# Optimization experiments

Measured on AMD Instinct MI355X. Metric: run time of the kernel, lower is better.

Reference implementation:

```python
import jax, jax.numpy as jnp
import numpy as np

B, N, E = 32, 128, 16384
D, H, O, A = 72, 72, 72, 4   # n_input, n_hidden, n_output, n_node_attr
C_WEIGHT = 1.0
EPS = 1e-5  # BatchNorm1d default eps


def setup_inputs() -> dict:
    key = jax.random.key(0)
    ks = jax.random.split(key, 16)
    rn = lambda k, shp, s=0.05: jax.random.normal(k, shp, jnp.float32) * s
    return {
        "h": jax.random.normal(ks[0], (B, N, D), jnp.float32),
        "x": jax.random.normal(ks[1], (B, N, 4), jnp.float32),
        "edgei": jax.random.randint(ks[2], (B, E), 0, N),
        "edgej": jax.random.randint(ks[3], (B, E), 0, N),
        "node_attr": jax.random.normal(ks[4], (B, N, A), jnp.float32),
        # phi_e: Linear(2D+2 -> H, no bias), BN, ReLU, Linear(H->H), ReLU
        "We1": rn(ks[5], (2 * D + 2, H)),
        "g1": jnp.ones((H,), jnp.float32), "b1": jnp.zeros((H,), jnp.float32),
        "We2": rn(ks[6], (H, H)), "be2": jnp.zeros((H,), jnp.float32),
        # phi_m: Linear(H->1), Sigmoid
        "Wm": rn(ks[7], (H, 1)), "bm": jnp.zeros((1,), jnp.float32),
        # phi_x: Linear(H->H), ReLU, Linear(H->1, no bias, tiny init)
        "Wx1": rn(ks[8], (H, H)), "bx1": jnp.zeros((H,), jnp.float32),
        "Wx2": rn(ks[9], (H, 1), 0.001),
        # phi_h: Linear(H+D+A -> H), BN, ReLU, Linear(H->O)
        "Wh1": rn(ks[10], (H + D + A, H)), "bh1": jnp.zeros((H,), jnp.float32),
        "gh": jnp.ones((H,), jnp.float32), "bh": jnp.zeros((H,), jnp.float32),
        "Wh2": rn(ks[11], (H, O)), "bh2": jnp.zeros((O,), jnp.float32),
    }


def _psi(p):
    return jnp.sign(p) * jnp.log1p(jnp.abs(p))


def _normsq4(p):  # Minkowski norm: p0^2 - p1^2 - p2^2 - p3^2
    psq = p * p
    return 2.0 * psq[..., 0] - psq.sum(axis=-1)


def _dotsq4(p, q):  # Minkowski inner product
    pq = p * q
    return 2.0 * pq[..., 0] - pq.sum(axis=-1)


def _batchnorm(z, g, b):  # training-mode BatchNorm1d over flattened batch dim
    mu = z.mean(axis=0)
    var = z.var(axis=0)
    return (z - mu) * jax.lax.rsqrt(var + EPS) * g + b


_seg_sum = jax.vmap(lambda d, s: jax.ops.segment_sum(d, s, num_segments=N))


def reference(h, x, edgei, edgej, node_attr,
              We1, g1, b1, We2, be2, Wm, bm,
              Wx1, bx1, Wx2, Wh1, bh1, gh, bh, Wh2, bh2):
    # gather edge endpoint features (equiv. to torch.gather along dim 1)
    xi = jnp.take_along_axis(x, edgei[:, :, None], axis=1)    # [B,E,4]
    xj = jnp.take_along_axis(x, edgej[:, :, None], axis=1)
    hi = jnp.take_along_axis(h, edgei[:, :, None], axis=1)    # [B,E,D]
    hj = jnp.take_along_axis(h, edgej[:, :, None], axis=1)
    x_diff = xi - xj
    norms = _psi(_normsq4(x_diff))[..., None]                 # [B,E,1]
    dots = _psi(_dotsq4(xi, xj))[..., None]                   # [B,E,1]

    # m_model: phi_e then sigmoid gate phi_m
    feat = jnp.concatenate([hi, hj, norms, dots], axis=-1)    # [B,E,2D+2]
    z = feat.reshape(-1, 2 * D + 2) @ We1
    z = jax.nn.relu(_batchnorm(z, g1, b1))
    z = jax.nn.relu(z @ We2 + be2)
    m = z.reshape(B, E, H)
    m = m * jax.nn.sigmoid(m @ Wm + bm)                       # gated messages

    # x_model: equivariant coordinate update (segment mean over edges)
    gate = jax.nn.relu(m @ Wx1 + bx1) @ Wx2                   # [B,E,1]
    trans = jnp.clip(x_diff * gate, -100.0, 100.0)
    agg = _seg_sum(trans, edgei)                              # [B,N,4]
    cnt = _seg_sum(jnp.ones_like(trans), edgei)
    x_out = x + (agg / jnp.maximum(cnt, 1.0)) * C_WEIGHT

    # h_model: segment sum of messages, node MLP, residual
    magg = _seg_sum(m, edgei)                                 # [B,N,H]
    hin = jnp.concatenate([h, magg, node_attr], axis=-1).reshape(-1, H + D + A)
    z2 = hin @ Wh1 + bh1
    z2 = jax.nn.relu(_batchnorm(z2, gh, bh))
    z2 = z2 @ Wh2 + bh2
    h_out = h + z2.reshape(B, N, O)

    return (h_out, x_out, m)
```

## Files before the change

kernel.cpp:

```cpp
#include <hip/hip_runtime.h>

#define BB 32
#define NN 128
#define EE 16384
#define ROWS_E (BB*EE)
#define ROWS_N (BB*NN)
#define EPS_BN 1e-5f

#define XOUT_OFF (ROWS_N*72)
#define M_OFF    (XOUT_OFF + ROWS_N*4)

#define ST1_OFF 0
#define ST2_OFF 512
#define AGG_OFF 1024
#define CNT_OFF (AGG_OFF + ROWS_N*4)
#define MAGG_OFF (CNT_OFF + ROWS_N)
#define Z2_OFF (MAGG_OFF + ROWS_N*72)
#define WB_OFF (Z2_OFF + ROWS_N*72)

#define WE1T_OFF 0
#define WE2T_OFF 13440
#define WX1T_OFF 21760
#define WH1T_OFF 30080
#define WH2T_OFF 43520
#define WB_TOTAL 51840
#define WAB_TOTAL 13824
#define PREP_TOTAL (WB_TOTAL + WAB_TOTAL)

typedef __attribute__((ext_vector_type(8))) short short8;
typedef __attribute__((ext_vector_type(4))) float f32x4;

__device__ __forceinline__ float psi_f(float p) {
    return copysignf(log1pf(fabsf(p)), p);
}
__device__ __forceinline__ unsigned pk(float a, float b) {
    unsigned r;
    asm("v_cvt_pk_bf16_f32 %0, %1, %2" : "=v"(r) : "v"(a), "v"(b));
    return r;
}
__device__ __forceinline__ unsigned short f2bf(float f) {
    unsigned r;
    asm("v_cvt_pk_bf16_f32 %0, %1, %1" : "=v"(r) : "v"(f));
    return (unsigned short)r;
}

__global__ void k_prep(const float* __restrict__ We1, const float* __restrict__ We2,
                       const float* __restrict__ Wx1, const float* __restrict__ Wh1,
                       const float* __restrict__ Wh2, unsigned short* __restrict__ wb,
                       unsigned short* __restrict__ wab)
{
    int idx = blockIdx.x * 256 + threadIdx.x;
    if (idx >= PREP_TOTAL) return;
    if (idx >= WB_TOTAL) {
        int off = idx - WB_TOTAL, n = off / 96, k = off % 96;
        float v = 0.f;
        if (k < 72) v = (n < 72) ? We1[k * 72 + n] : We1[(72 + k) * 72 + (n - 72)];
        wab[off] = f2bf(v);
        return;
    }
    const float* src; int off, n, k, K;
    if (idx < WE2T_OFF)      { off = idx;            n = off/168; k = off%168; src = We1; K = 146; }
    else if (idx < WH1T_OFF && idx >= WX1T_OFF) { off = idx - WX1T_OFF; n = off/104; k = off%104; src = Wx1; K = 72; }
    else if (idx < WX1T_OFF) { off = idx - WE2T_OFF; n = off/104; k = off%104; src = We2; K = 72; }
    else if (idx < WH2T_OFF) { off = idx - WH1T_OFF; n = off/168; k = off%168; src = Wh1; K = 148; }
    else                     { off = idx - WH2T_OFF; n = off/104; k = off%104; src = Wh2; K = 72; }
    float v = (n < 72 && k < K) ? src[k * 72 + n] : 0.f;
    wb[idx] = f2bf(v);
}

__global__ __launch_bounds__(256, 2) void k_ab(
    const float* __restrict__ h, const unsigned short* __restrict__ Wabt,
    float* __restrict__ ab)
{
    __shared__ unsigned short Hs[128 * 104];
    int tid = threadIdx.x;
    int rl = tid >> 1, half = tid & 1;
    size_t row = (size_t)blockIdx.x * 128 + rl;
    const float4* hp = (const float4*)(h + row * 72) + half * 9;
    uint2* hr = (uint2*)(&Hs[rl * 104 + half * 36]);
    #pragma unroll
    for (int q = 0; q < 9; q++) {
        float4 v = hp[q];
        hr[q] = make_uint2(pk(v.x, v.y), pk(v.z, v.w));
    }
    {
        uint2* zp = (uint2*)(&Hs[rl * 104 + 72 + half * 12]);
        zp[0] = make_uint2(0u, 0u); zp[1] = make_uint2(0u, 0u); zp[2] = make_uint2(0u, 0u);
    }
    int wv = tid >> 6, lane = tid & 63, c = lane & 15, quad = lane >> 4;
    f32x4 acc[2][9] = {};
    #pragma unroll
    for (int kc = 0; kc < 3; kc++) {
        int k0 = kc * 32 + quad * 8;
        short8 a0 = *(const short8*)(&Hs[(wv * 32 + c) * 104 + k0]);
        short8 a1 = *(const short8*)(&Hs[(wv * 32 + 16 + c) * 104 + k0]);
        #pragma unroll
        for (int ct = 0; ct < 9; ct++) {
            short8 bf = *(const short8*)(&Wabt[(ct * 16 + c) * 96 + k0]);
            acc[0][ct] = __builtin_amdgcn_mfma_f32_16x16x32_bf16(a0, bf, acc[0][ct], 0, 0, 0);
            acc[1][ct] = __builtin_amdgcn_mfma_f32_16x16x32_bf16(a1, bf, acc[1][ct], 0, 0, 0);
        }
    }
    size_t rbase = (size_t)blockIdx.x * 128 + wv * 32 + quad * 4;
    #pragma unroll
    for (int rt = 0; rt < 2; rt++)
        #pragma unroll
        for (int ct = 0; ct < 9; ct++) {
            int col = ct * 16 + c;
            #pragma unroll
            for (int r = 0; r < 4; r++)
                ab[(rbase + rt * 16 + r) * 144 + col] = acc[rt][ct][r];
        }
}

__global__ __launch_bounds__(288) void k_stats_lite(
    const float* __restrict__ ab, const float* __restrict__ x,
    const int* __restrict__ ei, const int* __restrict__ ej,
    const float* __restrict__ We1, float* __restrict__ st)
{
    __shared__ float uu[256], tt[256];
    __shared__ int iofs[256], jofs[256];
    __shared__ float ssum[4][72];
    __shared__ float ssq[4][72];
    int c = threadIdx.x, ty = threadIdx.y;
    int tf = ty * 72 + c;
    float al = We1[144 * 72 + c], be = We1[145 * 72 + c];
    float s = 0.f, q = 0.f;
    int ebase = blockIdx.x * 512;
    #pragma unroll
    for (int tile = 0; tile < 2; tile++) {
        if (tf < 256) {
            int e = ebase + tile * 256 + tf;
            int b = e >> 14;
            int i = ei[e], j = ej[e];
            float4 xi = *(const float4*)(x + (size_t)(b * 128 + i) * 4);
            float4 xj = *(const float4*)(x + (size_t)(b * 128 + j) * 4);
            float d0 = xi.x - xj.x, d1 = xi.y - xj.y, d2 = xi.z - xj.z, d3 = xi.w - xj.w;
            uu[tf] = psi_f(d0*d0 - d1*d1 - d2*d2 - d3*d3);
            tt[tf] = psi_f(xi.x*xj.x - xi.y*xj.y - xi.z*xj.z - xi.w*xj.w);
            iofs[tf] = (b * 128 + i) * 144;
            jofs[tf] = (b * 128 + j) * 144 + 72;
        }
        __syncthreads();
        #pragma unroll 4
        for (int k = 0; k < 64; k++) {
            int idx = ty * 64 + k;
            float av = ab[iofs[idx] + c];
            float bv = ab[jofs[idx] + c];
            float z = (av + bv) + (uu[idx] * al + tt[idx] * be);
            s += z; q += z * z;
        }
        __syncthreads();
    }
    ssum[ty][c] = s; ssq[ty][c] = q;
    __syncthreads();
    if (ty == 0) {
        s = ssum[0][c] + ssum[1][c] + ssum[2][c] + ssum[3][c];
        q = ssq[0][c] + ssq[1][c] + ssq[2][c] + ssq[3][c];
        atomicAdd(&st[c], s);
        atomicAdd(&st[72 + c], q);
    }
}

__global__ void k_finalize1(float* __restrict__ st, const float* __restrict__ g1,
                            const float* __restrict__ b1, float inv_rows)
{
    int c = threadIdx.x;
    if (c < 72) {
        float mean = st[c] * inv_rows;
        float var  = st[72 + c] * inv_rows - mean * mean;
        float sc = rsqrtf(var + EPS_BN) * g1[c];
        st[144 + c] = sc;
        st[216 + c] = b1[c] - mean * sc;
    }
}

__global__ void k_finalize(float* __restrict__ st, float inv_rows)
{
    int c = threadIdx.x;
    if (c < 72) {
        float mean = st[c] * inv_rows;
        float var  = st[72 + c] * inv_rows - mean * mean;
        st[144 + c] = mean;
        st[216 + c] = rsqrtf(var + EPS_BN);
    }
}

__global__ __launch_bounds__(256, 4) void k_edge_fused(
    const float* __restrict__ ab, const float* __restrict__ x,
    const int* __restrict__ ei, const int* __restrict__ ej,
    const float* __restrict__ We1, const float* __restrict__ st1,
    const float* __restrict__ be2, const float* __restrict__ Wm, const float* __restrict__ bm,
    const float* __restrict__ bx1, const float* __restrict__ Wx2,
    const unsigned short* __restrict__ We2t, const unsigned short* __restrict__ Wx1t,
    float* __restrict__ m, float* __restrict__ agg, float* __restrict__ cnt)
{
    __shared__ unsigned short Zt[128 * 104];
    __shared__ float g2buf[128];
    int tid = threadIdx.x;
    int rl = tid >> 1, half = tid & 1;
    size_t row = (size_t)blockIdx.x * 128 + rl;
    int b = (int)(row >> 14);
    int i = ei[row], j = ej[row];
    float4 xi = *(const float4*)(x + (size_t)(b * 128 + i) * 4);
    float4 xj = *(const float4*)(x + (size_t)(b * 128 + j) * 4);
    float d0 = xi.x - xj.x, d1 = xi.y - xj.y, d2 = xi.z - xj.z, d3 = xi.w - xj.w;
    float u = psi_f(d0*d0 - d1*d1 - d2*d2 - d3*d3);
    float t = psi_f(xi.x*xj.x - xi.y*xj.y - xi.z*xj.z - xi.w*xj.w);
    const float4* ar  = (const float4*)(ab + (size_t)(b * 128 + i) * 144 + half * 36);
    const float4* br  = (const float4*)(ab + (size_t)(b * 128 + j) * 144 + 72 + half * 36);
    const float4* alp = (const float4*)(We1 + 144 * 72 + half * 36);
    const float4* bep = (const float4*)(We1 + 145 * 72 + half * 36);
    const float4* scp = (const float4*)(st1 + 144 + half * 36);
    const float4* shp = (const float4*)(st1 + 216 + half * 36);
    uint2* zrow = (uint2*)(&Zt[rl * 104 + half * 36]);
    #pragma unroll
    for (int q = 0; q < 9; q++) {
        float4 av = ar[q], bv = br[q], al = alp[q], be = bep[q], sc = scp[q], sh = shp[q];
        float z0 = fmaxf((av.x + bv.x + u * al.x + t * be.x) * sc.x + sh.x, 0.f);
        float z1 = fmaxf((av.y + bv.y + u * al.y + t * be.y) * sc.y + sh.y, 0.f);
        float z2 = fmaxf((av.z + bv.z + u * al.z + t * be.z) * sc.z + sh.z, 0.f);
        float z3 = fmaxf((av.w + bv.w + u * al.w + t * be.w) * sc.w + sh.w, 0.f);
        zrow[q] = make_uint2(pk(z0, z1), pk(z2, z3));
    }
    {
        uint2* zp = (uint2*)(&Zt[rl * 104 + 72 + half * 12]);
        zp[0] = make_uint2(0u, 0u); zp[1] = make_uint2(0u, 0u); zp[2] = make_uint2(0u, 0u);
    }

    int wv = tid >> 6, lane = tid & 63, c = lane & 15, quad = lane >> 4;
    f32x4 acc2[2][5] = {};
    #pragma unroll
    for (int kc = 0; kc < 3; kc++) {
        int k0 = kc * 32 + quad * 8;
        short8 a0 = *(const short8*)(&Zt[(wv * 32 + c) * 104 + k0]);
        short8 a1 = *(const short8*)(&Zt[(wv * 32 + 16 + c) * 104 + k0]);
        #pragma unroll
        for (int ct = 0; ct < 5; ct++) {
            short8 bf = *(const short8*)(&We2t[(ct * 16 + c) * 104 + k0]);
            acc2[0][ct] = __builtin_amdgcn_mfma_f32_16x16x32_bf16(a0, bf, acc2[0][ct], 0, 0, 0);
            acc2[1][ct] = __builtin_amdgcn_mfma_f32_16x16x32_bf16(a1, bf, acc2[1][ct], 0, 0, 0);
        }
    }
    float part[2][4] = {};
    float bm0 = bm[0];
    #pragma unroll
    for (int ct = 0; ct < 5; ct++) {
        int col = ct * 16 + c;
        float bias = (col < 72) ? be2[col] : 0.f;
        float wm   = (col < 72) ? Wm[col]  : 0.f;
        #pragma unroll
        for (int rt = 0; rt < 2; rt++)
            #pragma unroll
            for (int r = 0; r < 4; r++) {
                float tv = fmaxf(acc2[rt][ct][r] + bias, 0.f);
                acc2[rt][ct][r] = tv;
                part[rt][r] += tv * wm;
            }
    }
    float sg[2][4];
    #pragma unroll
    for (int rt = 0; rt < 2; rt++)
        #pragma unroll
        for (int r = 0; r < 4; r++) {
            float s = part[rt][r];
            s += __shfl_xor(s, 1); s += __shfl_xor(s, 2);
            s += __shfl_xor(s, 4); s += __shfl_xor(s, 8);
            sg[rt][r] = 1.f / (1.f + expf(-(s + bm0)));
        }
    size_t rbase = (size_t)blockIdx.x * 128 + wv * 32 + quad * 4;
    #pragma unroll
    for (int rt = 0; rt < 2; rt++)
        #pragma unroll
        for (int ct = 0; ct < 5; ct++) {
            int col = ct * 16 + c;
            #pragma unroll
            for (int r = 0; r < 4; r++) {
                float mv = acc2[rt][ct][r] * sg[rt][r];
                int lrow = wv * 32 + rt * 16 + quad * 4 + r;
                Zt[lrow * 104 + col] = f2bf(mv);
                if (col < 72) m[(rbase + rt * 16 + r) * 72 + col] = mv;
            }
        }
    f32x4 acc3[2][5] = {};
    #pragma unroll
    for (int kc = 0; kc < 3; kc++) {
        int k0 = kc * 32 + quad * 8;
        short8 a0 = *(const short8*)(&Zt[(wv * 32 + c) * 104 + k0]);
        short8 a1 = *(const short8*)(&Zt[(wv * 32 + 16 + c) * 104 + k0]);
        #pragma unroll
        for (int ct = 0; ct < 5; ct++) {
            short8 bf = *(const short8*)(&Wx1t[(ct * 16 + c) * 104 + k0]);
            acc3[0][ct] = __builtin_amdgcn_mfma_f32_16x16x32_bf16(a0, bf, acc3[0][ct], 0, 0, 0);
            acc3[1][ct] = __builtin_amdgcn_mfma_f32_16x16x32_bf16(a1, bf, acc3[1][ct], 0, 0, 0);
        }
    }
    float part3[2][4] = {};
    #pragma unroll
    for (int ct = 0; ct < 5; ct++) {
        int col = ct * 16 + c;
        float bias = (col < 72) ? bx1[col] : 0.f;
        float wx   = (col < 72) ? Wx2[col] : 0.f;
        #pragma unroll
        for (int rt = 0; rt < 2; rt++)
            #pragma unroll
            for (int r = 0; r < 4; r++)
                part3[rt][r] += fmaxf(acc3[rt][ct][r] + bias, 0.f) * wx;
    }
    #pragma unroll
    for (int rt = 0; rt < 2; rt++)
        #pragma unroll
        for (int r = 0; r < 4; r++) {
            float s = part3[rt][r];
            s += __shfl_xor(s, 1); s += __shfl_xor(s, 2);
            s += __shfl_xor(s, 4); s += __shfl_xor(s, 8);
            if (c == 0) g2buf[wv * 32 + rt * 16 + quad * 4 + r] = s;
        }
    __syncthreads();
    if (tid < 128) {
        size_t erow = (size_t)blockIdx.x * 128 + tid;
        int b2 = (int)(erow >> 14);
        int i2 = ei[erow], j2 = ej[erow];
        float g2 = g2buf[tid];
        float4 xi2 = *(const float4*)(x + (size_t)(b2 * 128 + i2) * 4);
        float4 xj2 = *(const float4*)(x + (size_t)(b2 * 128 + j2) * 4);
        float t0 = fminf(fmaxf((xi2.x - xj2.x) * g2, -100.f), 100.f);
        float t1 = fminf(fmaxf((xi2.y - xj2.y) * g2, -100.f), 100.f);
        float t2 = fminf(fmaxf((xi2.z - xj2.z) * g2, -100.f), 100.f);
        float t3 = fminf(fmaxf((xi2.w - xj2.w) * g2, -100.f), 100.f);
        float* ap = agg + (size_t)(b2 * 128 + i2) * 4;
        atomicAdd(ap + 0, t0); atomicAdd(ap + 1, t1);
        atomicAdd(ap + 2, t2); atomicAdd(ap + 3, t3);
        atomicAdd(cnt + (size_t)(b2 * 128 + i2), 1.f);
    }
}

__global__ __launch_bounds__(256, 4) void k_magg(
    const float* __restrict__ m, const int* __restrict__ ei, float* __restrict__ magg)
{
    __shared__ float accum[128 * 72];
    int tid = threadIdx.x;
    for (int q = tid; q < 9216; q += 256) accum[q] = 0.f;
    __syncthreads();
    int b = blockIdx.x >> 5, chunk = blockIdx.x & 31;
    int wv = tid >> 6, lane = tid & 63;
    int ebase = b * 16384 + chunk * 512;
    for (int e = wv; e < 512; e += 8) {
        int e0 = ebase + e, e1 = ebase + e + 4;
        int n0 = ei[e0], n1 = ei[e1];
        const float* r0 = m + (size_t)e0 * 72;
        const float* r1 = m + (size_t)e1 * 72;
        float v0 = r0[lane];
        float v1 = r1[lane];
        float t0 = (lane < 8) ? r0[64 + lane] : 0.f;
        float t1 = (lane < 8) ? r1[64 + lane] : 0.f;
        atomicAdd(&accum[n0 * 72 + lane], v0);
        if (lane < 8) atomicAdd(&accum[n0 * 72 + 64 + lane], t0);
        atomicAdd(&accum[n1 * 72 + lane], v1);
        if (lane < 8) atomicAdd(&accum[n1 * 72 + 64 + lane], t1);
    }
    __syncthreads();
    float* mg = magg + (size_t)b * 9216;
    for (int q = tid; q < 9216; q += 256) atomicAdd(&mg[q], accum[q]);
}

__global__ __launch_bounds__(256) void k_node_gemm1(
    const float* __restrict__ h, const float* __restrict__ node_attr,
    const float* __restrict__ magg, const unsigned short* __restrict__ Wh1t,
    const float* __restrict__ bh1, float* __restrict__ z2, float* __restrict__ st)
{
    __shared__ unsigned short At[128 * 168];
    __shared__ unsigned short Wt[80 * 168];
    __shared__ float sred[4][144];
    int tid = threadIdx.x;
    {
        const uint4* s = (const uint4*)Wh1t; uint4* d = (uint4*)Wt;
        for (int q = tid; q < 1680; q += 256) d[q] = s[q];
    }
    int rl = tid >> 1, half = tid & 1;
    size_t row = (size_t)blockIdx.x * 128 + rl;
    const float4* sp = (const float4*)((half ? magg : h) + row * 72);
    uint2* arow = (uint2*)(&At[rl * 168 + half * 72]);
    #pragma unroll
    for (int q = 0; q < 18; q++) {
        float4 v = sp[q];
        arow[q] = make_uint2(pk(v.x, v.y), pk(v.z, v.w));
    }
    if (half) {
        float4 na = *(const float4*)(node_attr + row * 4);
        *(unsigned*)(&At[rl * 168 + 144]) = pk(na.x, na.y);
        *(unsigned*)(&At[rl * 168 + 146]) = pk(na.z, na.w);
        unsigned* tailp = (unsigned*)(&At[rl * 168 + 148]);
        #pragma unroll
        for (int q = 0; q < 10; q++) tailp[q] = 0u;
    }
    __syncthreads();

    int wv = tid >> 6, lane = tid & 63, c = lane & 15, quad = lane >> 4;
    f32x4 acc[2][5] = {};
    #pragma unroll
    for (int kc = 0; kc < 5; kc++) {
        int k0 = kc * 32 + quad * 8;
        short8 a0 = *(const short8*)(&At[(wv * 32 + c) * 168 + k0]);
        short8 a1 = *(const short8*)(&At[(wv * 32 + 16 + c) * 168 + k0]);
        #pragma unroll
        for (int ct = 0; ct < 5; ct++) {
            short8 bf = *(const short8*)(&Wt[(ct * 16 + c) * 168 + k0]);
            acc[0][ct] = __builtin_amdgcn_mfma_f32_16x16x32_bf16(a0, bf, acc[0][ct], 0, 0, 0);
            acc[1][ct] = __builtin_amdgcn_mfma_f32_16x16x32_bf16(a1, bf, acc[1][ct], 0, 0, 0);
        }
    }
    size_t rbase = (size_t)blockIdx.x * 128 + wv * 32 + quad * 4;
    #pragma unroll
    for (int ct = 0; ct < 5; ct++) {
        int col = ct * 16 + c;
        float bias = (col < 72) ? bh1[col] : 0.f;
        float s = 0.f, q = 0.f;
        #pragma unroll
        for (int rt = 0; rt < 2; rt++) {
            float* op = z2 + (rbase + rt * 16) * 72 + col;
            #pragma unroll
            for (int r = 0; r < 4; r++) {
                float v = acc[rt][ct][r] + bias;
                if (col < 72) op[(size_t)r * 72] = v;
                s += v; q += v * v;
            }
        }
        s += __shfl_xor(s, 16); s += __shfl_xor(s, 32);
        q += __shfl_xor(q, 16); q += __shfl_xor(q, 32);
        if (lane < 16 && col < 72) { sred[wv][col] = s; sred[wv][72 + col] = q; }
    }
    __syncthreads();
    if (tid < 144)
        atomicAdd(&st[tid], sred[0][tid] + sred[1][tid] + sred[2][tid] + sred[3][tid]);
}

__global__ __launch_bounds__(256) void k_node_final(
    const float* __restrict__ h, const float* __restrict__ x,
    const float* __restrict__ z2, const float* __restrict__ st2,
    const float* __restrict__ gh, const float* __restrict__ bh,
    const unsigned short* __restrict__ Wh2t, const float* __restrict__ bh2,
    const float* __restrict__ agg, const float* __restrict__ cnt,
    float* __restrict__ hout, float* __restrict__ xout)
{
    __shared__ unsigned short Zt[128 * 104];
    __shared__ unsigned short Wt[80 * 104];
    int tid = threadIdx.x;
    {
        const uint4* s = (const uint4*)Wh2t; uint4* d = (uint4*)Wt;
        for (int q = tid; q < 1040; q += 256) d[q] = s[q];
    }
    int rl = tid >> 1, half = tid & 1;
    size_t row = (size_t)blockIdx.x * 128 + rl;
    const float* mean = st2 + 144;
    const float* inv  = st2 + 216;
    const float4* zp = (const float4*)(z2 + row * 72) + half * 9;
    uint2* arow = (uint2*)(&Zt[rl * 104 + half * 36]);
    #pragma unroll
    for (int q = 0; q < 9; q++) {
        int k = half * 36 + q * 4;
        float4 v = zp[q];
        float a0 = fmaxf((v.x - mean[k  ]) * inv[k  ] * gh[k  ] + bh[k  ], 0.f);
        float a1 = fmaxf((v.y - mean[k+1]) * inv[k+1] * gh[k+1] + bh[k+1], 0.f);
        float a2 = fmaxf((v.z - mean[k+2]) * inv[k+2] * gh[k+2] + bh[k+2], 0.f);
        float a3 = fmaxf((v.w - mean[k+3]) * inv[k+3] * gh[k+3] + bh[k+3], 0.f);
        arow[q] = make_uint2(pk(a0, a1), pk(a2, a3));
    }
    uint2* prow = (uint2*)(&Zt[rl * 104]);
    #pragma unroll
    for (int q = 0; q < 4; q++) prow[18 + half * 4 + q] = make_uint2(0u, 0u);
    __syncthreads();

    int wv = tid >> 6, lane = tid & 63, c = lane & 15, quad = lane >> 4;
    f32x4 acc[2][5] = {};
    #pragma unroll
    for (int kc = 0; kc < 3; kc++) {
        int k0 = kc * 32 + quad * 8;
        short8 a0 = *(const short8*)(&Zt[(wv * 32 + c) * 104 + k0]);
        short8 a1 = *(const short8*)(&Zt[(wv * 32 + 16 + c) * 104 + k0]);
        #pragma unroll
        for (int ct = 0; ct < 5; ct++) {
            short8 bf = *(const short8*)(&Wt[(ct * 16 + c) * 104 + k0]);
            acc[0][ct] = __builtin_amdgcn_mfma_f32_16x16x32_bf16(a0, bf, acc[0][ct], 0, 0, 0);
            acc[1][ct] = __builtin_amdgcn_mfma_f32_16x16x32_bf16(a1, bf, acc[1][ct], 0, 0, 0);
        }
    }
    size_t rbase = (size_t)blockIdx.x * 128 + wv * 32 + quad * 4;
    #pragma unroll
    for (int rt = 0; rt < 2; rt++)
        #pragma unroll
        for (int ct = 0; ct < 5; ct++) {
            int col = ct * 16 + c;
            if (col < 72) {
                float bias = bh2[col];
                #pragma unroll
                for (int r = 0; r < 4; r++) {
                    size_t gr = (rbase + rt * 16 + r);
                    hout[gr * 72 + col] = h[gr * 72 + col] + acc[rt][ct][r] + bias;
                }
            }
        }
    if (tid < 128) {
        size_t nrow = (size_t)blockIdx.x * 128 + tid;
        float cn = fmaxf(cnt[nrow], 1.f);
        float4 ag = *(const float4*)(agg + nrow * 4);
        float4 xv = *(const float4*)(x + nrow * 4);
        ((float4*)xout)[nrow] = make_float4(xv.x + ag.x / cn, xv.y + ag.y / cn,
                                            xv.z + ag.z / cn, xv.w + ag.w / cn);
    }
}

extern "C" void kernel_launch(void* const* d_in, const int* in_sizes, int n_in,
                              void* d_out, int out_size, void* d_ws, size_t ws_size,
                              hipStream_t stream)
{
    const float* h   = (const float*)d_in[0];
    const float* x   = (const float*)d_in[1];
    const int*   ei  = (const int*)d_in[2];
    const int*   ej  = (const int*)d_in[3];
    const float* na  = (const float*)d_in[4];
    const float* We1 = (const float*)d_in[5];
    const float* g1  = (const float*)d_in[6];
    const float* b1  = (const float*)d_in[7];
    const float* We2 = (const float*)d_in[8];
    const float* be2 = (const float*)d_in[9];
    const float* Wm  = (const float*)d_in[10];
    const float* bm  = (const float*)d_in[11];
    const float* Wx1 = (const float*)d_in[12];
    const float* bx1 = (const float*)d_in[13];
    const float* Wx2 = (const float*)d_in[14];
    const float* Wh1 = (const float*)d_in[15];
    const float* bh1 = (const float*)d_in[16];
    const float* gh  = (const float*)d_in[17];
    const float* bhp = (const float*)d_in[18];
    const float* Wh2 = (const float*)d_in[19];
    const float* bh2 = (const float*)d_in[20];

    float* out  = (float*)d_out;
    float* hout = out;
    float* xout = out + XOUT_OFF;
    float* m    = out + M_OFF;
    float* ws   = (float*)d_ws;
    float* st1  = ws + ST1_OFF;
    float* st2  = ws + ST2_OFF;
    float* agg  = ws + AGG_OFF;
    float* cnt  = ws + CNT_OFF;
    float* magg = ws + MAGG_OFF;
    float* z2   = ws + Z2_OFF;
    unsigned short* wb = (unsigned short*)(ws + WB_OFF);
    float* ab = ws + MAGG_OFF;
    unsigned short* wab = (unsigned short*)xout;

    hipMemsetAsync(d_ws, 0, (size_t)MAGG_OFF * sizeof(float), stream);
    k_prep<<<(PREP_TOTAL + 255) / 256, 256, 0, stream>>>(We1, We2, Wx1, Wh1, Wh2, wb, wab);
    k_ab<<<ROWS_N / 128, 256, 0, stream>>>(h, wab, ab);
    k_stats_lite<<<1024, dim3(72, 4), 0, stream>>>(ab, x, ei, ej, We1, st1);
    k_finalize1<<<1, 128, 0, stream>>>(st1, g1, b1, 1.0f / (float)ROWS_E);
    k_edge_fused<<<ROWS_E / 128, 256, 0, stream>>>(ab, x, ei, ej, We1, st1, be2, Wm, bm,
                                                   bx1, Wx2, wb + WE2T_OFF, wb + WX1T_OFF,
                                                   m, agg, cnt);
    hipMemsetAsync(magg, 0, (size_t)(ROWS_N * 72) * sizeof(float), stream);
    k_magg<<<1024, 256, 0, stream>>>(m, ei, magg);
    k_node_gemm1<<<ROWS_N / 128, 256, 0, stream>>>(h, na, magg, wb + WH1T_OFF, bh1, z2, st2);
    k_finalize<<<1, 128, 0, stream>>>(st2, 1.0f / (float)ROWS_N);
    k_node_final<<<ROWS_N / 128, 256, 0, stream>>>(h, x, z2, st2, gh, bhp,
                                                   wb + WH2T_OFF, bh2, agg, cnt, hout, xout);
}
```

Measured before the change: 638.6 us.

## Swizzle block indices across XCDs, split stats blocks, unroll magg, raise occupancy

Remaps block indices in the stats, edge and magg kernels so that consecutive blocks land on the same XCD (blockIdx & 7 striding). The aim is for blocks that touch the same batch's ab/x/m rows to share an L2. The stats kernel now handles 256 edges per block across 2048 blocks instead of looping over two tiles, which exposes more parallelism at the cost of twice as many global atomics. The edge kernel's launch bound asks for 6 blocks per CU, which may cap registers and cause spills. The magg loop is unrolled to four edges per iteration to raise memory-level parallelism.

Result: slower. 767.7 us (+20.2%).

```diff
diff --git a/kernel.cpp b/kernel.cpp
--- a/kernel.cpp
+++ b/kernel.cpp
@@ -124,33 +124,30 @@
     __shared__ float ssq[4][72];
     int c = threadIdx.x, ty = threadIdx.y;
     int tf = ty * 72 + c;
+    int bidx = (blockIdx.x & 7) * 256 + (blockIdx.x >> 3);
     float al = We1[144 * 72 + c], be = We1[145 * 72 + c];
     float s = 0.f, q = 0.f;
-    int ebase = blockIdx.x * 512;
-    #pragma unroll
-    for (int tile = 0; tile < 2; tile++) {
-        if (tf < 256) {
-            int e = ebase + tile * 256 + tf;
-            int b = e >> 14;
-            int i = ei[e], j = ej[e];
-            float4 xi = *(const float4*)(x + (size_t)(b * 128 + i) * 4);
-            float4 xj = *(const float4*)(x + (size_t)(b * 128 + j) * 4);
-            float d0 = xi.x - xj.x, d1 = xi.y - xj.y, d2 = xi.z - xj.z, d3 = xi.w - xj.w;
-            uu[tf] = psi_f(d0*d0 - d1*d1 - d2*d2 - d3*d3);
-            tt[tf] = psi_f(xi.x*xj.x - xi.y*xj.y - xi.z*xj.z - xi.w*xj.w);
-            iofs[tf] = (b * 128 + i) * 144;
-            jofs[tf] = (b * 128 + j) * 144 + 72;
-        }
-        __syncthreads();
-        #pragma unroll 4
-        for (int k = 0; k < 64; k++) {
-            int idx = ty * 64 + k;
-            float av = ab[iofs[idx] + c];
-            float bv = ab[jofs[idx] + c];
-            float z = (av + bv) + (uu[idx] * al + tt[idx] * be);
-            s += z; q += z * z;
-        }
-        __syncthreads();
+    int ebase = bidx * 256;
+    if (tf < 256) {
+        int e = ebase + tf;
+        int b = e >> 14;
+        int i = ei[e], j = ej[e];
+        float4 xi = *(const float4*)(x + (size_t)(b * 128 + i) * 4);
+        float4 xj = *(const float4*)(x + (size_t)(b * 128 + j) * 4);
+        float d0 = xi.x - xj.x, d1 = xi.y - xj.y, d2 = xi.z - xj.z, d3 = xi.w - xj.w;
+        uu[tf] = psi_f(d0*d0 - d1*d1 - d2*d2 - d3*d3);
+        tt[tf] = psi_f(xi.x*xj.x - xi.y*xj.y - xi.z*xj.z - xi.w*xj.w);
+        iofs[tf] = (b * 128 + i) * 144;
+        jofs[tf] = (b * 128 + j) * 144 + 72;
+    }
+    __syncthreads();
+    #pragma unroll 4
+    for (int k = 0; k < 64; k++) {
+        int idx = ty * 64 + k;
+        float av = ab[iofs[idx] + c];
+        float bv = ab[jofs[idx] + c];
+        float z = (av + bv) + (uu[idx] * al + tt[idx] * be);
+        s += z; q += z * z;
     }
     ssum[ty][c] = s; ssq[ty][c] = q;
     __syncthreads();
@@ -186,7 +183,7 @@
     }
 }
 
-__global__ __launch_bounds__(256, 4) void k_edge_fused(
+__global__ __launch_bounds__(256, 6) void k_edge_fused(
     const float* __restrict__ ab, const float* __restrict__ x,
     const int* __restrict__ ei, const int* __restrict__ ej,
     const float* __restrict__ We1, const float* __restrict__ st1,
@@ -198,8 +195,9 @@
     __shared__ unsigned short Zt[128 * 104];
     __shared__ float g2buf[128];
     int tid = threadIdx.x;
+    int bidx = (blockIdx.x & 7) * 512 + (blockIdx.x >> 3);
     int rl = tid >> 1, half = tid & 1;
-    size_t row = (size_t)blockIdx.x * 128 + rl;
+    size_t row = (size_t)bidx * 128 + rl;
     int b = (int)(row >> 14);
     int i = ei[row], j = ej[row];
     float4 xi = *(const float4*)(x + (size_t)(b * 128 + i) * 4);
@@ -268,7 +266,7 @@
             s += __shfl_xor(s, 4); s += __shfl_xor(s, 8);
             sg[rt][r] = 1.f / (1.f + expf(-(s + bm0)));
         }
-    size_t rbase = (size_t)blockIdx.x * 128 + wv * 32 + quad * 4;
+    size_t rbase = (size_t)bidx * 128 + wv * 32 + quad * 4;
     #pragma unroll
     for (int rt = 0; rt < 2; rt++)
         #pragma unroll
@@ -318,7 +316,7 @@
         }
     __syncthreads();
     if (tid < 128) {
-        size_t erow = (size_t)blockIdx.x * 128 + tid;
+        size_t erow = (size_t)bidx * 128 + tid;
         int b2 = (int)(erow >> 14);
         int i2 = ei[erow], j2 = ej[erow];
         float g2 = g2buf[tid];
@@ -342,22 +340,30 @@
     int tid = threadIdx.x;
     for (int q = tid; q < 9216; q += 256) accum[q] = 0.f;
     __syncthreads();
-    int b = blockIdx.x >> 5, chunk = blockIdx.x & 31;
+    int bidx = (blockIdx.x & 7) * 128 + (blockIdx.x >> 3);
+    int b = bidx >> 5, chunk = bidx & 31;
     int wv = tid >> 6, lane = tid & 63;
     int ebase = b * 16384 + chunk * 512;
-    for (int e = wv; e < 512; e += 8) {
-        int e0 = ebase + e, e1 = ebase + e + 4;
-        int n0 = ei[e0], n1 = ei[e1];
+    for (int e = wv; e < 512; e += 16) {
+        int e0 = ebase + e, e1 = ebase + e + 4, e2 = ebase + e + 8, e3 = ebase + e + 12;
+        int n0 = ei[e0], n1 = ei[e1], n2 = ei[e2], n3 = ei[e3];
         const float* r0 = m + (size_t)e0 * 72;
         const float* r1 = m + (size_t)e1 * 72;
-        float v0 = r0[lane];
-        float v1 = r1[lane];
+        const float* r2 = m + (size_t)e2 * 72;
+        const float* r3 = m + (size_t)e3 * 72;
+        float v0 = r0[lane], v1 = r1[lane], v2 = r2[lane], v3 = r3[lane];
         float t0 = (lane < 8) ? r0[64 + lane] : 0.f;
         float t1 = (lane < 8) ? r1[64 + lane] : 0.f;
+        float t2 = (lane < 8) ? r2[64 + lane] : 0.f;
+        float t3 = (lane < 8) ? r3[64 + lane] : 0.f;
         atomicAdd(&accum[n0 * 72 + lane], v0);
         if (lane < 8) atomicAdd(&accum[n0 * 72 + 64 + lane], t0);
         atomicAdd(&accum[n1 * 72 + lane], v1);
         if (lane < 8) atomicAdd(&accum[n1 * 72 + 64 + lane], t1);
+        atomicAdd(&accum[n2 * 72 + lane], v2);
+        if (lane < 8) atomicAdd(&accum[n2 * 72 + 64 + lane], t2);
+        atomicAdd(&accum[n3 * 72 + lane], v3);
+        if (lane < 8) atomicAdd(&accum[n3 * 72 + 64 + lane], t3);
     }
     __syncthreads();
     float* mg = magg + (size_t)b * 9216;
@@ -554,7 +560,7 @@
     hipMemsetAsync(d_ws, 0, (size_t)MAGG_OFF * sizeof(float), stream);
     k_prep<<<(PREP_TOTAL + 255) / 256, 256, 0, stream>>>(We1, We2, Wx1, Wh1, Wh2, wb, wab);
     k_ab<<<ROWS_N / 128, 256, 0, stream>>>(h, wab, ab);
-    k_stats_lite<<<1024, dim3(72, 4), 0, stream>>>(ab, x, ei, ej, We1, st1);
+    k_stats_lite<<<2048, dim3(72, 4), 0, stream>>>(ab, x, ei, ej, We1, st1);
     k_finalize1<<<1, 128, 0, stream>>>(st1, g1, b1, 1.0f / (float)ROWS_E);
     k_edge_fused<<<ROWS_E / 128, 256, 0, stream>>>(ab, x, ei, ej, We1, st1, be2, Wm, bm,
                                                    bx1, Wx2, wb + WE2T_OFF, wb + WX1T_OFF,
```
